# Kernel tuning notes

Measured on AMD Instinct MI355X. Metric: run time of the kernel, lower is better.

The kernel has to match this reference:

```python
import jax, jax.numpy as jnp
import numpy as np

B, T, F, D, HD = 16, 512, 16, 256, 256


def _init(k, shape, fan_in):
    return (jax.random.uniform(k, shape, minval=-1.0, maxval=1.0) / np.sqrt(fan_in)).astype(jnp.float32)


def setup_inputs() -> dict:
    key = jax.random.key(0)
    ks = jax.random.split(key, 16)
    return {
        "x": jax.random.normal(ks[0], (B, T, F), dtype=jnp.float32),
        # per-variable encoder params, batched over F (Linear(1,D) + GRN(D,HD,D))
        "w1": _init(ks[1], (F, D), 1), "b1": _init(ks[2], (F, D), 1),
        "fc1_w": _init(ks[3], (F, D, HD), D), "fc1_b": _init(ks[4], (F, HD), D),
        "fc2_w": _init(ks[5], (F, HD, D), HD), "fc2_b": _init(ks[6], (F, D), HD),
        "glu_w": _init(ks[7], (F, D, 2 * D), D), "glu_b": _init(ks[8], (F, 2 * D), D),
        "ln_g": jnp.ones((F, D), jnp.float32), "ln_b": jnp.zeros((F, D), jnp.float32),
        # weight GRN(F, HD, F); skip is Identity since d_in == d_out
        "wg_fc1_w": _init(ks[9], (F, HD), F), "wg_fc1_b": _init(ks[10], (HD,), F),
        "wg_fc2_w": _init(ks[11], (HD, F), HD), "wg_fc2_b": _init(ks[12], (F,), HD),
        "wg_glu_w": _init(ks[13], (F, 2 * F), F), "wg_glu_b": _init(ks[14], (2 * F,), F),
        "wg_ln_g": jnp.ones((F,), jnp.float32), "wg_ln_b": jnp.zeros((F,), jnp.float32),
    }


def _layernorm(x, g, b, eps=1e-5):
    m = jnp.mean(x, axis=-1, keepdims=True)
    v = jnp.var(x, axis=-1, keepdims=True)
    return (x - m) * jax.lax.rsqrt(v + eps) * g + b


def reference(x, w1, b1, fc1_w, fc1_b, fc2_w, fc2_b, glu_w, glu_b, ln_g, ln_b,
              wg_fc1_w, wg_fc1_b, wg_fc2_w, wg_fc2_b, wg_glu_w, wg_glu_b,
              wg_ln_g, wg_ln_b):
    # --- per-variable towers, batched over F (dropout is identity at eval) ---
    h0 = jax.nn.relu(x[..., None] * w1 + b1)                       # [B,T,F,D]
    y = jax.nn.elu(jnp.einsum('btfd,fdh->btfh', h0, fc1_w) + fc1_b)
    y = jnp.einsum('btfh,fhd->btfd', y, fc2_w) + fc2_b
    g = jnp.einsum('btfd,fde->btfe', y, glu_w) + glu_b             # [B,T,F,2D]
    a, gate = jnp.split(g, 2, axis=-1)
    H = _layernorm(h0 + a * jax.nn.sigmoid(gate), ln_g, ln_b)      # [B,T,F,D]
    # --- variable-weight GRN (time_distributed=True) ---
    yw = jax.nn.elu(x @ wg_fc1_w + wg_fc1_b)
    yw = yw @ wg_fc2_w + wg_fc2_b
    gw = x @ jnp.zeros((F, 0), x.dtype) if False else yw @ wg_glu_w + wg_glu_b
    aw, gatew = jnp.split(gw, 2, axis=-1)
    w = _layernorm(x + aw * jax.nn.sigmoid(gatew), wg_ln_g, wg_ln_b)
    w = jax.nn.softmax(w, axis=-1)                                 # [B,T,F]
    z = jnp.einsum('btfd,btf->btd', H, w)                          # [B,T,D]
    return z, w
```

## Files before the change

kernel.cpp:

```cpp
#include <hip/hip_runtime.h>
#include <hip/hip_bf16.h>

#define NBT 8192
#define NF  16
#define ND  256
#define NH  256
#define N2D 512

typedef short bf16x8 __attribute__((ext_vector_type(8)));
typedef float f32x4 __attribute__((ext_vector_type(4)));
typedef unsigned short u16x8 __attribute__((ext_vector_type(8)));

__device__ __forceinline__ float bf2f(unsigned short u) {
  return __uint_as_float(((unsigned)u) << 16);
}
__device__ __forceinline__ unsigned short f2bf(float f) {
  unsigned u = __float_as_uint(f);
  return (unsigned short)((u + 0x7FFFu + ((u >> 16) & 1u)) >> 16);
}

#define GLOAD16(src, dst)                                                     \
  __builtin_amdgcn_global_load_lds(                                           \
      (const __attribute__((address_space(1))) unsigned int*)(src),           \
      (__attribute__((address_space(3))) unsigned int*)(dst), 16, 0, 0)

__global__ __launch_bounds__(256) void wgrn_kernel(
    const float* __restrict__ x, const float* __restrict__ fw1,
    const float* __restrict__ fb1, const float* __restrict__ fw2,
    const float* __restrict__ fb2, const float* __restrict__ gwt,
    const float* __restrict__ gbt, const float* __restrict__ lng,
    const float* __restrict__ lnb, float* __restrict__ wout) {
  __shared__ float w1t[256 * 16];
  __shared__ float w2s[256 * 16];
  const int tid = threadIdx.x;
  for (int i = tid; i < 4096; i += 256) {
    int ff = i >> 8, j = i & 255;
    w1t[j * 16 + ff] = fw1[i];
    w2s[i] = fw2[i];
  }
  __syncthreads();
  const int sub  = tid & 7;
  const int rowi = tid >> 3;
  const int bt   = blockIdx.x * 32 + rowi;
  float xr[16];
#pragma unroll
  for (int i = 0; i < 4; ++i)
    *(float4*)&xr[i * 4] = *(const float4*)(x + (size_t)bt * 16 + i * 4);
  float acc2[16];
#pragma unroll
  for (int q = 0; q < 16; ++q) acc2[q] = 0.f;
  for (int j = sub; j < 256; j += 8) {
    float h = fb1[j];
    const float* wr = &w1t[j * 16];
#pragma unroll
    for (int q = 0; q < 16; ++q) h = fmaf(xr[q], wr[q], h);
    h = h > 0.f ? h : expm1f(h);
    const float* w2r = &w2s[j * 16];
#pragma unroll
    for (int q = 0; q < 16; ++q) acc2[q] = fmaf(h, w2r[q], acc2[q]);
  }
#pragma unroll
  for (int off = 1; off < 8; off <<= 1) {
#pragma unroll
    for (int q = 0; q < 16; ++q) acc2[q] += __shfl_xor(acc2[q], off);
  }
#pragma unroll
  for (int q = 0; q < 16; ++q) acc2[q] += fb2[q];
  float gw[32];
#pragma unroll
  for (int k = 0; k < 32; ++k) {
    float s = gbt[k];
#pragma unroll
    for (int q = 0; q < 16; ++q) s = fmaf(acc2[q], gwt[q * 32 + k], s);
    gw[k] = s;
  }
  float v[16];
  float mean = 0.f;
#pragma unroll
  for (int q = 0; q < 16; ++q) {
    float sg = 1.f / (1.f + __expf(-gw[16 + q]));
    v[q] = fmaf(gw[q], sg, xr[q]);
    mean += v[q];
  }
  mean *= (1.f / 16.f);
  float var = 0.f;
#pragma unroll
  for (int q = 0; q < 16; ++q) { float d = v[q] - mean; var = fmaf(d, d, var); }
  var *= (1.f / 16.f);
  float rstd = rsqrtf(var + 1e-5f);
  float mx = -1e30f;
#pragma unroll
  for (int q = 0; q < 16; ++q) {
    v[q] = (v[q] - mean) * rstd * lng[q] + lnb[q];
    mx = fmaxf(mx, v[q]);
  }
  float se = 0.f;
#pragma unroll
  for (int q = 0; q < 16; ++q) { v[q] = __expf(v[q] - mx); se += v[q]; }
  float inv = 1.f / se;
  if (sub == 0) {
#pragma unroll
    for (int i = 0; i < 4; ++i) {
      float4 o = { v[i*4+0]*inv, v[i*4+1]*inv, v[i*4+2]*inv, v[i*4+3]*inv };
      *(float4*)(wout + (size_t)bt * 16 + i * 4) = o;
    }
  }
}

__global__ void transpose_cast(const float* __restrict__ src,
                               unsigned short* __restrict__ dst, int K, int N) {
  __shared__ float tile[32][33];
  const int f = blockIdx.z;
  const float* s = src + (size_t)f * K * N;
  unsigned short* d = dst + (size_t)f * K * N;
  const int k0 = blockIdx.y * 32, n0 = blockIdx.x * 32;
  const int tx = threadIdx.x, ty = threadIdx.y;
#pragma unroll
  for (int i = 0; i < 32; i += 8)
    tile[ty + i][tx] = s[(size_t)(k0 + ty + i) * N + n0 + tx];
  __syncthreads();
#pragma unroll
  for (int i = 0; i < 32; i += 8)
    d[(size_t)(n0 + ty + i) * K + k0 + tx] = f2bf(tile[tx][ty + i]);
}

__global__ __launch_bounds__(256, 4) void g1_kernel(
    const float* __restrict__ x, const float* __restrict__ w1,
    const float* __restrict__ b1, const unsigned short* __restrict__ fc1t,
    const float* __restrict__ fc1_b, unsigned short* __restrict__ y1) {
  __shared__ __align__(16) char arena[34816];
  __shared__ float xw[128];
  unsigned short* abuf = (unsigned short*)arena;
  unsigned short* bbuf = (unsigned short*)(arena + 17408);
  unsigned short* cbuf = (unsigned short*)arena;
  const int tid = threadIdx.x, lane = tid & 63, wid = tid >> 6;
  const int rl = lane & 15, kc = lane >> 4;
  const int f = blockIdx.z, m0 = blockIdx.y * 128, n0 = blockIdx.x * 128;
  const unsigned short* Bf = fc1t + (size_t)f * NH * ND;
  const float* w1f = w1 + f * ND;
  const float* b1f = b1 + f * ND;
  if (tid < 128) xw[tid] = x[(size_t)(m0 + tid) * NF + f];
  const int wm = (wid >> 1) * 64, wn = (wid & 1) * 64;

  f32x4 acc[4][4];
#pragma unroll
  for (int m = 0; m < 4; ++m)
#pragma unroll
    for (int n = 0; n < 4; ++n) acc[m][n] = (f32x4){0.f, 0.f, 0.f, 0.f};

  for (int kt = 0; kt < ND; kt += 64) {
    __syncthreads();
#pragma unroll
    for (int i = 0; i < 4; ++i) {
      int s = tid + 256 * i;
      int row = s >> 3, sl = s & 7;
      const unsigned short* gb =
          Bf + (size_t)(n0 + row) * ND + kt + ((sl ^ (row & 7)) << 3);
      GLOAD16(gb, (char*)bbuf + (wid * 64 + 256 * i) * 16);
    }
#pragma unroll
    for (int i = 0; i < 4; ++i) {
      int vi = tid + 256 * i;
      int row = vi >> 3, c8 = vi & 7, c = kt + c8 * 8;
      float xv = xw[row];
      float4 wa = *(const float4*)(w1f + c);
      float4 wb = *(const float4*)(w1f + c + 4);
      float4 ba = *(const float4*)(b1f + c);
      float4 bb = *(const float4*)(b1f + c + 4);
      u16x8 o;
      o[0] = f2bf(fmaxf(fmaf(xv, wa.x, ba.x), 0.f));
      o[1] = f2bf(fmaxf(fmaf(xv, wa.y, ba.y), 0.f));
      o[2] = f2bf(fmaxf(fmaf(xv, wa.z, ba.z), 0.f));
      o[3] = f2bf(fmaxf(fmaf(xv, wa.w, ba.w), 0.f));
      o[4] = f2bf(fmaxf(fmaf(xv, wb.x, bb.x), 0.f));
      o[5] = f2bf(fmaxf(fmaf(xv, wb.y, bb.y), 0.f));
      o[6] = f2bf(fmaxf(fmaf(xv, wb.z, bb.z), 0.f));
      o[7] = f2bf(fmaxf(fmaf(xv, wb.w, bb.w), 0.f));
      *(u16x8*)(abuf + row * 68 + c8 * 8) = o;
    }
    __syncthreads();
#pragma unroll
    for (int kk = 0; kk < 2; ++kk) {
      bf16x8 av[4], bv[4];
      int s = kk * 4 + kc;
#pragma unroll
      for (int m = 0; m < 4; ++m) {
        int r = wm + m * 16 + rl;
        av[m] = *(const bf16x8*)(abuf + r * 68 + s * 8);
      }
#pragma unroll
      for (int n = 0; n < 4; ++n) {
        int rr = wn + n * 16 + rl;
        int ps = s ^ (rr & 7);
        bv[n] = *(const bf16x8*)((const char*)bbuf + rr * 128 + ps * 16);
      }
#pragma unroll
      for (int m = 0; m < 4; ++m)
#pragma unroll
        for (int n = 0; n < 4; ++n)
          acc[m][n] = __builtin_amdgcn_mfma_f32_16x16x32_bf16(av[m], bv[n],
                                                              acc[m][n], 0, 0, 0);
    }
  }

  __syncthreads();
  const int rq = lane >> 4;
#pragma unroll
  for (int n = 0; n < 4; ++n) {
    int cl = wn + n * 16 + rl;
    float bvv = fc1_b[f * NH + n0 + cl];
#pragma unroll
    for (int m = 0; m < 4; ++m) {
#pragma unroll
      for (int j = 0; j < 4; ++j) {
        int r = wm + m * 16 + rq * 4 + j;
        float v = acc[m][n][j] + bvv;
        v = v > 0.f ? v : expm1f(v);
        cbuf[r * 136 + cl] = f2bf(v);
      }
    }
  }
  __syncthreads();
#pragma unroll
  for (int v = 0; v < 8; ++v) {
    int row = (tid >> 4) + v * 16, chunk = tid & 15;
    u16x8 val = *(const u16x8*)(cbuf + row * 136 + chunk * 8);
    *(u16x8*)(y1 + ((size_t)f * NBT + m0 + row) * NH + n0 + chunk * 8) = val;
  }
}

__global__ __launch_bounds__(512, 4) void g2_kernel(
    const unsigned short* __restrict__ y1,
    const unsigned short* __restrict__ fc2t, const float* __restrict__ fc2_b,
    unsigned short* __restrict__ y2) {
  __shared__ __align__(16) char arena[49152];
  unsigned short* abuf = (unsigned short*)arena;
  unsigned short* bbuf = (unsigned short*)(arena + 16384);
  unsigned short* cbuf = (unsigned short*)arena;
  const int tid = threadIdx.x, lane = tid & 63, wid = tid >> 6;
  const int rl = lane & 15, kc = lane >> 4;
  const int f = blockIdx.y, m0 = blockIdx.x * 128;
  const unsigned short* Af = y1 + (size_t)f * NBT * NH;
  const unsigned short* Bf = fc2t + (size_t)f * ND * NH;
  const int wm = (wid >> 2) * 64, wn = (wid & 3) * 64;

  f32x4 acc[4][4];
#pragma unroll
  for (int m = 0; m < 4; ++m)
#pragma unroll
    for (int n = 0; n < 4; ++n) acc[m][n] = (f32x4){0.f, 0.f, 0.f, 0.f};

  for (int kt = 0; kt < NH; kt += 64) {
    __syncthreads();
#pragma unroll
    for (int i = 0; i < 2; ++i) {
      int s = tid + 512 * i;
      int row = s >> 3, sl = s & 7;
      const unsigned short* ga =
          Af + (size_t)(m0 + row) * NH + kt + ((sl ^ (row & 7)) << 3);
      GLOAD16(ga, (char*)abuf + (wid * 64 + 512 * i) * 16);
    }
#pragma unroll
    for (int i = 0; i < 4; ++i) {
      int s = tid + 512 * i;
      int row = s >> 3, sl = s & 7;
      const unsigned short* gb =
          Bf + (size_t)row * NH + kt + ((sl ^ (row & 7)) << 3);
      GLOAD16(gb, (char*)bbuf + (wid * 64 + 512 * i) * 16);
    }
    __syncthreads();
#pragma unroll
    for (int kk = 0; kk < 2; ++kk) {
      bf16x8 av[4], bv[4];
      int s = kk * 4 + kc;
#pragma unroll
      for (int m = 0; m < 4; ++m) {
        int r = wm + m * 16 + rl;
        int ps = s ^ (r & 7);
        av[m] = *(const bf16x8*)((const char*)abuf + r * 128 + ps * 16);
      }
#pragma unroll
      for (int n = 0; n < 4; ++n) {
        int rr = wn + n * 16 + rl;
        int ps = s ^ (rr & 7);
        bv[n] = *(const bf16x8*)((const char*)bbuf + rr * 128 + ps * 16);
      }
#pragma unroll
      for (int m = 0; m < 4; ++m)
#pragma unroll
        for (int n = 0; n < 4; ++n)
          acc[m][n] = __builtin_amdgcn_mfma_f32_16x16x32_bf16(av[m], bv[n],
                                                              acc[m][n], 0, 0, 0);
    }
  }

  const int rq = lane >> 4;
  const int hsel = (wid & 3) >> 1;
#pragma unroll
  for (int h = 0; h < 2; ++h) {
    __syncthreads();
    if (hsel == h) {
#pragma unroll
      for (int n = 0; n < 4; ++n) {
        int c = wn + n * 16 + rl;
        int cl = c - h * 128;
        float bvv = fc2_b[f * ND + c];
#pragma unroll
        for (int m = 0; m < 4; ++m) {
#pragma unroll
          for (int j = 0; j < 4; ++j) {
            int r = wm + m * 16 + rq * 4 + j;
            cbuf[r * 136 + cl] = f2bf(acc[m][n][j] + bvv);
          }
        }
      }
    }
    __syncthreads();
#pragma unroll
    for (int v = 0; v < 4; ++v) {
      int row = (tid >> 4) + v * 32, chunk = tid & 15;
      u16x8 val = *(const u16x8*)(cbuf + row * 136 + chunk * 8);
      *(u16x8*)(y2 + ((size_t)f * NBT + m0 + row) * ND + h * 128 + chunk * 8) =
          val;
    }
  }
}

__global__ __launch_bounds__(512, 4) void g3_kernel(
    const unsigned short* __restrict__ y2,
    const unsigned short* __restrict__ glut, const float* __restrict__ glu_b,
    const float* __restrict__ x, const float* __restrict__ w1,
    const float* __restrict__ b1, const float* __restrict__ ln_g,
    const float* __restrict__ ln_b, unsigned short* __restrict__ H) {
  __shared__ __align__(16) char arena[73728];
  __shared__ float xw[64];
  __shared__ float2 sums[8][64];
  __shared__ float2 sums2[64];
  unsigned short* abuf = (unsigned short*)arena;
  unsigned short* bbuf = (unsigned short*)(arena + 8192);
  unsigned short* vbuf = (unsigned short*)arena;

  const int tid = threadIdx.x, lane = tid & 63, wid = tid >> 6;
  const int rl = lane & 15, rq = lane >> 4;
  const int f = blockIdx.y, m0 = blockIdx.x * 64;
  const unsigned short* Af = y2 + (size_t)f * NBT * ND;
  const unsigned short* Bf = glut + (size_t)f * ND * N2D;
  const float* w1f = w1 + f * ND;
  const float* b1f = b1 + f * ND;
  const int colb = wid * 32;
  if (tid < 64) xw[tid] = x[(size_t)(m0 + tid) * NF + f];

  f32x4 acc[4][4];
#pragma unroll
  for (int m = 0; m < 4; ++m)
#pragma unroll
    for (int n = 0; n < 4; ++n) acc[m][n] = (f32x4){0.f, 0.f, 0.f, 0.f};

  for (int kt = 0; kt < ND; kt += 64) {
    __syncthreads();
    {
      int s = tid;
      int row = s >> 3, sl = s & 7;
      const unsigned short* ga =
          Af + (size_t)(m0 + row) * ND + kt + ((sl ^ (row & 7)) << 3);
      GLOAD16(ga, (char*)abuf + (wid * 64) * 16);
    }
#pragma unroll
    for (int i = 0; i < 8; ++i) {
      int s = tid + 512 * i;
      int row = s >> 3, sl = s & 7;
      const unsigned short* gb =
          Bf + (size_t)row * ND + kt + ((sl ^ (row & 7)) << 3);
      GLOAD16(gb, (char*)bbuf + (wid * 64 + 512 * i) * 16);
    }
    __syncthreads();
#pragma unroll
    for (int kk = 0; kk < 2; ++kk) {
      bf16x8 av[4], bv[4];
      int s = kk * 4 + rq;
#pragma unroll
      for (int m = 0; m < 4; ++m) {
        int r = m * 16 + rl;
        int ps = s ^ (r & 7);
        av[m] = *(const bf16x8*)((const char*)abuf + r * 128 + ps * 16);
      }
#pragma unroll
      for (int n = 0; n < 4; ++n) {
        int rr = (n < 2) ? (colb + n * 16 + rl)
                         : (256 + colb + (n - 2) * 16 + rl);
        int ps = s ^ (rr & 7);
        bv[n] = *(const bf16x8*)((const char*)bbuf + rr * 128 + ps * 16);
      }
#pragma unroll
      for (int m = 0; m < 4; ++m)
#pragma unroll
        for (int n = 0; n < 4; ++n)
          acc[m][n] = __builtin_amdgcn_mfma_f32_16x16x32_bf16(av[m], bv[n],
                                                              acc[m][n], 0, 0, 0);
    }
  }

#pragma unroll
  for (int n = 0; n < 2; ++n) {
    int cA = colb + n * 16 + rl;
    float ab_ = glu_b[f * N2D + cA];
    float gb_ = glu_b[f * N2D + 256 + cA];
    float w1c = w1f[cA], b1c = b1f[cA];
#pragma unroll
    for (int m = 0; m < 4; ++m) {
#pragma unroll
      for (int j = 0; j < 4; ++j) {
        int r = m * 16 + rq * 4 + j;
        float a = acc[m][n][j] + ab_;
        float g = acc[m][n + 2][j] + gb_;
        float sg = 1.f / (1.f + __expf(-g));
        float h0 = fmaxf(fmaf(xw[r], w1c, b1c), 0.f);
        acc[m][n][j] = fmaf(a, sg, h0);
      }
    }
  }
#pragma unroll
  for (int m = 0; m < 4; ++m) {
#pragma unroll
    for (int j = 0; j < 4; ++j) {
      float s = acc[m][0][j] + acc[m][1][j];
      float q = fmaf(acc[m][0][j], acc[m][0][j],
                     acc[m][1][j] * acc[m][1][j]);
#pragma unroll
      for (int off = 1; off < 16; off <<= 1) {
        s += __shfl_xor(s, off);
        q += __shfl_xor(q, off);
      }
      if (rl == 0) sums[wid][m * 16 + rq * 4 + j] = make_float2(s, q);
    }
  }
  __syncthreads();
  if (tid < 64) {
    float tot = 0.f, tot2 = 0.f;
#pragma unroll
    for (int wv = 0; wv < 8; ++wv) {
      float2 p = sums[wv][tid];
      tot += p.x;
      tot2 += p.y;
    }
    float mean = tot * (1.f / 256.f);
    float var  = tot2 * (1.f / 256.f) - mean * mean;
    sums2[tid] = make_float2(mean, rsqrtf(var + 1e-5f));
  }
  __syncthreads();
#pragma unroll
  for (int n = 0; n < 2; ++n) {
    int cA = colb + n * 16 + rl;
    float lg = ln_g[f * ND + cA], lb = ln_b[f * ND + cA];
#pragma unroll
    for (int m = 0; m < 4; ++m) {
#pragma unroll
      for (int j = 0; j < 4; ++j) {
        int r = m * 16 + rq * 4 + j;
        float2 mr = sums2[r];
        vbuf[r * 264 + cA] = f2bf(fmaf((acc[m][n][j] - mr.x) * mr.y, lg, lb));
      }
    }
  }
  __syncthreads();
  {
    int row = tid >> 3, chunk = tid & 7;
    unsigned short* Hrow = H + ((size_t)f * NBT + m0 + row) * ND;
#pragma unroll
    for (int v = 0; v < 4; ++v) {
      u16x8 val = *(const u16x8*)(vbuf + row * 264 + chunk * 8 + v * 64);
      *(u16x8*)(Hrow + chunk * 8 + v * 64) = val;
    }
  }
}

__global__ __launch_bounds__(256) void combine_kernel(
    const unsigned short* __restrict__ H, const float* __restrict__ w,
    float* __restrict__ z) {
  int idx = blockIdx.x * 256 + threadIdx.x;
  int bt = idx >> 5;
  int d  = (idx & 31) << 3;
  float a[8];
#pragma unroll
  for (int j = 0; j < 8; ++j) a[j] = 0.f;
#pragma unroll
  for (int f = 0; f < 16; ++f) {
    u16x8 hv = *(const u16x8*)(H + ((size_t)f * NBT + bt) * ND + d);
    float wvv = w[bt * 16 + f];
#pragma unroll
    for (int j = 0; j < 8; ++j) a[j] = fmaf(bf2f(hv[j]), wvv, a[j]);
  }
  float4 o0 = {a[0], a[1], a[2], a[3]};
  float4 o1 = {a[4], a[5], a[6], a[7]};
  *(float4*)(z + (size_t)bt * ND + d)     = o0;
  *(float4*)(z + (size_t)bt * ND + d + 4) = o1;
}

extern "C" void kernel_launch(void* const* d_in, const int* in_sizes, int n_in,
                              void* d_out, int out_size, void* d_ws,
                              size_t ws_size, hipStream_t stream) {
  const float* x        = (const float*)d_in[0];
  const float* w1       = (const float*)d_in[1];
  const float* b1       = (const float*)d_in[2];
  const float* fc1_w    = (const float*)d_in[3];
  const float* fc1_b    = (const float*)d_in[4];
  const float* fc2_w    = (const float*)d_in[5];
  const float* fc2_b    = (const float*)d_in[6];
  const float* glu_w    = (const float*)d_in[7];
  const float* glu_b    = (const float*)d_in[8];
  const float* ln_g     = (const float*)d_in[9];
  const float* ln_b     = (const float*)d_in[10];
  const float* wg_fc1_w = (const float*)d_in[11];
  const float* wg_fc1_b = (const float*)d_in[12];
  const float* wg_fc2_w = (const float*)d_in[13];
  const float* wg_fc2_b = (const float*)d_in[14];
  const float* wg_glu_w = (const float*)d_in[15];
  const float* wg_glu_b = (const float*)d_in[16];
  const float* wg_ln_g  = (const float*)d_in[17];
  const float* wg_ln_b  = (const float*)d_in[18];

  char* ws = (char*)d_ws;
  unsigned short* fc1t = (unsigned short*)ws;
  unsigned short* fc2t = fc1t + (size_t)NF * NH * ND;
  unsigned short* glut = fc2t + (size_t)NF * ND * NH;
  unsigned short* y1   = (unsigned short*)(ws + (8ull << 20));
  unsigned short* y2   = (unsigned short*)(ws + (72ull << 20));
  unsigned short* Hbuf = (unsigned short*)(ws + (136ull << 20));

  float* zout = (float*)d_out;
  float* wout = zout + (size_t)NBT * ND;

  wgrn_kernel<<<256, 256, 0, stream>>>(x, wg_fc1_w, wg_fc1_b, wg_fc2_w,
                                       wg_fc2_b, wg_glu_w, wg_glu_b, wg_ln_g,
                                       wg_ln_b, wout);
  transpose_cast<<<dim3(8, 8, NF),  dim3(32, 8), 0, stream>>>(fc1_w, fc1t, ND, NH);
  transpose_cast<<<dim3(8, 8, NF),  dim3(32, 8), 0, stream>>>(fc2_w, fc2t, NH, ND);
  transpose_cast<<<dim3(16, 8, NF), dim3(32, 8), 0, stream>>>(glu_w, glut, ND, N2D);

  g1_kernel<<<dim3(NH / 128, NBT / 128, NF), 256, 0, stream>>>(
      x, w1, b1, fc1t, fc1_b, y1);
  g2_kernel<<<dim3(NBT / 128, NF), 512, 0, stream>>>(y1, fc2t, fc2_b, y2);
  g3_kernel<<<dim3(NBT / 64, NF), 512, 0, stream>>>(y2, glut, glu_b, x, w1, b1,
                                                    ln_g, ln_b, Hbuf);
  combine_kernel<<<(NBT * ND / 8) / 256, 256, 0, stream>>>(Hbuf, wout, zout);

  (void)in_sizes; (void)n_in; (void)out_size; (void)ws_size;
}
```

Before: 232.1 us.

## Double-buffer LDS tiles in GEMM kernels and merge weight transpose launches

Restructures the K loops of the three per-variable GEMM kernels into a two-stage ping-pong pipeline. The next tile's global-to-LDS loads (and, in g1, the h0 recompute) are issued before the MFMAs on the current tile, which also removes one barrier per iteration. The aim is to hide global load latency behind compute. In exchange the LDS footprint doubles (up to about 147KB in g3), which cuts how many blocks fit per CU and lowers the launch_bounds occupancy hints. The three weight transpose/cast launches are merged into one kernel to save launch overhead, at the cost of some duplicated or idle blocks.

```diff
diff --git a/kernel.cpp b/kernel.cpp
--- a/kernel.cpp
+++ b/kernel.cpp
@@ -107,13 +107,26 @@
   }
 }
 
-__global__ void transpose_cast(const float* __restrict__ src,
-                               unsigned short* __restrict__ dst, int K, int N) {
+__global__ void transpose_all(const float* __restrict__ fc1_w,
+                              const float* __restrict__ fc2_w,
+                              const float* __restrict__ glu_w,
+                              unsigned short* __restrict__ fc1t,
+                              unsigned short* __restrict__ fc2t,
+                              unsigned short* __restrict__ glut) {
   __shared__ float tile[32][33];
-  const int f = blockIdx.z;
+  const int which = blockIdx.z >> 4;
+  const int f     = blockIdx.z & 15;
+  const float* src;
+  unsigned short* dst;
+  int K, N, bx = blockIdx.x;
+  if (which == 0)      { src = fc1_w; dst = fc1t; K = ND; N = NH; }
+  else if (which == 1) { src = fc2_w; dst = fc2t; K = NH; N = ND; }
+  else                 { src = glu_w; dst = glut; K = ND; N = N2D;
+                         bx += (which == 3) ? 8 : 0; }
+  if (bx * 32 >= N) return;
   const float* s = src + (size_t)f * K * N;
   unsigned short* d = dst + (size_t)f * K * N;
-  const int k0 = blockIdx.y * 32, n0 = blockIdx.x * 32;
+  const int k0 = blockIdx.y * 32, n0 = bx * 32;
   const int tx = threadIdx.x, ty = threadIdx.y;
 #pragma unroll
   for (int i = 0; i < 32; i += 8)
@@ -124,23 +137,25 @@
     d[(size_t)(n0 + ty + i) * K + k0 + tx] = f2bf(tile[tx][ty + i]);
 }
 
-__global__ __launch_bounds__(256, 4) void g1_kernel(
+__global__ __launch_bounds__(256, 2) void g1_kernel(
     const float* __restrict__ x, const float* __restrict__ w1,
     const float* __restrict__ b1, const unsigned short* __restrict__ fc1t,
     const float* __restrict__ fc1_b, unsigned short* __restrict__ y1) {
-  __shared__ __align__(16) char arena[34816];
+  __shared__ __align__(16) char arena[67584];
   __shared__ float xw[128];
-  unsigned short* abuf = (unsigned short*)arena;
-  unsigned short* bbuf = (unsigned short*)(arena + 17408);
-  unsigned short* cbuf = (unsigned short*)arena;
+  unsigned short* abufs = (unsigned short*)arena;
+  unsigned short* bbufs = (unsigned short*)(arena + 34816);
+  unsigned short* cbuf  = (unsigned short*)arena;
   const int tid = threadIdx.x, lane = tid & 63, wid = tid >> 6;
   const int rl = lane & 15, kc = lane >> 4;
   const int f = blockIdx.z, m0 = blockIdx.y * 128, n0 = blockIdx.x * 128;
   const unsigned short* Bf = fc1t + (size_t)f * NH * ND;
   const float* w1f = w1 + f * ND;
   const float* b1f = b1 + f * ND;
+  const int wm = (wid >> 1) * 64, wn = (wid & 1) * 64;
+
   if (tid < 128) xw[tid] = x[(size_t)(m0 + tid) * NF + f];
-  const int wm = (wid >> 1) * 64, wn = (wid & 1) * 64;
+  __syncthreads();
 
   f32x4 acc[4][4];
 #pragma unroll
@@ -148,16 +163,19 @@
 #pragma unroll
     for (int n = 0; n < 4; ++n) acc[m][n] = (f32x4){0.f, 0.f, 0.f, 0.f};
 
-  for (int kt = 0; kt < ND; kt += 64) {
-    __syncthreads();
+  auto stage_B = [&](int kt, int buf) {
+    unsigned short* bb = bbufs + buf * (128 * 64);
 #pragma unroll
     for (int i = 0; i < 4; ++i) {
       int s = tid + 256 * i;
       int row = s >> 3, sl = s & 7;
       const unsigned short* gb =
           Bf + (size_t)(n0 + row) * ND + kt + ((sl ^ (row & 7)) << 3);
-      GLOAD16(gb, (char*)bbuf + (wid * 64 + 256 * i) * 16);
-    }
+      GLOAD16(gb, (char*)bb + (wid * 64 + 256 * i) * 16);
+    }
+  };
+  auto stage_h0 = [&](int kt, int buf) {
+    unsigned short* ab = abufs + buf * (128 * 68);
 #pragma unroll
     for (int i = 0; i < 4; ++i) {
       int vi = tid + 256 * i;
@@ -166,19 +184,22 @@
       float4 wa = *(const float4*)(w1f + c);
       float4 wb = *(const float4*)(w1f + c + 4);
       float4 ba = *(const float4*)(b1f + c);
-      float4 bb = *(const float4*)(b1f + c + 4);
+      float4 bb2 = *(const float4*)(b1f + c + 4);
       u16x8 o;
       o[0] = f2bf(fmaxf(fmaf(xv, wa.x, ba.x), 0.f));
       o[1] = f2bf(fmaxf(fmaf(xv, wa.y, ba.y), 0.f));
       o[2] = f2bf(fmaxf(fmaf(xv, wa.z, ba.z), 0.f));
       o[3] = f2bf(fmaxf(fmaf(xv, wa.w, ba.w), 0.f));
-      o[4] = f2bf(fmaxf(fmaf(xv, wb.x, bb.x), 0.f));
-      o[5] = f2bf(fmaxf(fmaf(xv, wb.y, bb.y), 0.f));
-      o[6] = f2bf(fmaxf(fmaf(xv, wb.z, bb.z), 0.f));
-      o[7] = f2bf(fmaxf(fmaf(xv, wb.w, bb.w), 0.f));
-      *(u16x8*)(abuf + row * 68 + c8 * 8) = o;
-    }
-    __syncthreads();
+      o[4] = f2bf(fmaxf(fmaf(xv, wb.x, bb2.x), 0.f));
+      o[5] = f2bf(fmaxf(fmaf(xv, wb.y, bb2.y), 0.f));
+      o[6] = f2bf(fmaxf(fmaf(xv, wb.z, bb2.z), 0.f));
+      o[7] = f2bf(fmaxf(fmaf(xv, wb.w, bb2.w), 0.f));
+      *(u16x8*)(ab + row * 68 + c8 * 8) = o;
+    }
+  };
+  auto compute = [&](int buf) {
+    const unsigned short* ab = abufs + buf * (128 * 68);
+    const unsigned short* bb = bbufs + buf * (128 * 64);
 #pragma unroll
     for (int kk = 0; kk < 2; ++kk) {
       bf16x8 av[4], bv[4];
@@ -186,13 +207,13 @@
 #pragma unroll
       for (int m = 0; m < 4; ++m) {
         int r = wm + m * 16 + rl;
-        av[m] = *(const bf16x8*)(abuf + r * 68 + s * 8);
+        av[m] = *(const bf16x8*)(ab + r * 68 + s * 8);
       }
 #pragma unroll
       for (int n = 0; n < 4; ++n) {
         int rr = wn + n * 16 + rl;
         int ps = s ^ (rr & 7);
-        bv[n] = *(const bf16x8*)((const char*)bbuf + rr * 128 + ps * 16);
+        bv[n] = *(const bf16x8*)((const char*)bb + rr * 128 + ps * 16);
       }
 #pragma unroll
       for (int m = 0; m < 4; ++m)
@@ -201,9 +222,20 @@
           acc[m][n] = __builtin_amdgcn_mfma_f32_16x16x32_bf16(av[m], bv[n],
                                                               acc[m][n], 0, 0, 0);
     }
-  }
-
-  __syncthreads();
+  };
+
+  stage_B(0, 0);
+  stage_h0(0, 0);
+  __syncthreads();
+#pragma unroll
+  for (int t = 0; t < 4; ++t) {
+    int cur = t & 1;
+    if (t < 3) stage_B((t + 1) * 64, cur ^ 1);
+    compute(cur);
+    if (t < 3) stage_h0((t + 1) * 64, cur ^ 1);
+    __syncthreads();
+  }
+
   const int rq = lane >> 4;
 #pragma unroll
   for (int n = 0; n < 4; ++n) {
@@ -229,14 +261,14 @@
   }
 }
 
-__global__ __launch_bounds__(512, 4) void g2_kernel(
+__global__ __launch_bounds__(512, 2) void g2_kernel(
     const unsigned short* __restrict__ y1,
     const unsigned short* __restrict__ fc2t, const float* __restrict__ fc2_b,
     unsigned short* __restrict__ y2) {
-  __shared__ __align__(16) char arena[49152];
-  unsigned short* abuf = (unsigned short*)arena;
-  unsigned short* bbuf = (unsigned short*)(arena + 16384);
-  unsigned short* cbuf = (unsigned short*)arena;
+  __shared__ __align__(16) char arena[98304];
+  unsigned short* abufs = (unsigned short*)arena;
+  unsigned short* bbufs = (unsigned short*)(arena + 32768);
+  unsigned short* cbuf  = (unsigned short*)arena;
   const int tid = threadIdx.x, lane = tid & 63, wid = tid >> 6;
   const int rl = lane & 15, kc = lane >> 4;
   const int f = blockIdx.y, m0 = blockIdx.x * 128;
@@ -250,15 +282,16 @@
 #pragma unroll
     for (int n = 0; n < 4; ++n) acc[m][n] = (f32x4){0.f, 0.f, 0.f, 0.f};
 
-  for (int kt = 0; kt < NH; kt += 64) {
-    __syncthreads();
+  auto stage = [&](int kt, int buf) {
+    unsigned short* ab = abufs + buf * (128 * 64);
+    unsigned short* bb = bbufs + buf * (256 * 64);
 #pragma unroll
     for (int i = 0; i < 2; ++i) {
       int s = tid + 512 * i;
       int row = s >> 3, sl = s & 7;
       const unsigned short* ga =
           Af + (size_t)(m0 + row) * NH + kt + ((sl ^ (row & 7)) << 3);
-      GLOAD16(ga, (char*)abuf + (wid * 64 + 512 * i) * 16);
+      GLOAD16(ga, (char*)ab + (wid * 64 + 512 * i) * 16);
     }
 #pragma unroll
     for (int i = 0; i < 4; ++i) {
@@ -266,9 +299,12 @@
       int row = s >> 3, sl = s & 7;
       const unsigned short* gb =
           Bf + (size_t)row * NH + kt + ((sl ^ (row & 7)) << 3);
-      GLOAD16(gb, (char*)bbuf + (wid * 64 + 512 * i) * 16);
-    }
-    __syncthreads();
+      GLOAD16(gb, (char*)bb + (wid * 64 + 512 * i) * 16);
+    }
+  };
+  auto compute = [&](int buf) {
+    const unsigned short* ab = abufs + buf * (128 * 64);
+    const unsigned short* bb = bbufs + buf * (256 * 64);
 #pragma unroll
     for (int kk = 0; kk < 2; ++kk) {
       bf16x8 av[4], bv[4];
@@ -277,13 +313,13 @@
       for (int m = 0; m < 4; ++m) {
         int r = wm + m * 16 + rl;
         int ps = s ^ (r & 7);
-        av[m] = *(const bf16x8*)((const char*)abuf + r * 128 + ps * 16);
+        av[m] = *(const bf16x8*)((const char*)ab + r * 128 + ps * 16);
       }
 #pragma unroll
       for (int n = 0; n < 4; ++n) {
         int rr = wn + n * 16 + rl;
         int ps = s ^ (rr & 7);
-        bv[n] = *(const bf16x8*)((const char*)bbuf + rr * 128 + ps * 16);
+        bv[n] = *(const bf16x8*)((const char*)bb + rr * 128 + ps * 16);
       }
 #pragma unroll
       for (int m = 0; m < 4; ++m)
@@ -292,13 +328,23 @@
           acc[m][n] = __builtin_amdgcn_mfma_f32_16x16x32_bf16(av[m], bv[n],
                                                               acc[m][n], 0, 0, 0);
     }
+  };
+
+  stage(0, 0);
+  __syncthreads();
+#pragma unroll
+  for (int t = 0; t < 4; ++t) {
+    int cur = t & 1;
+    if (t < 3) stage((t + 1) * 64, cur ^ 1);
+    compute(cur);
+    __syncthreads();
   }
 
   const int rq = lane >> 4;
   const int hsel = (wid & 3) >> 1;
 #pragma unroll
   for (int h = 0; h < 2; ++h) {
-    __syncthreads();
+    if (h) __syncthreads();
     if (hsel == h) {
 #pragma unroll
       for (int n = 0; n < 4; ++n) {
@@ -326,19 +372,19 @@
   }
 }
 
-__global__ __launch_bounds__(512, 4) void g3_kernel(
+__global__ __launch_bounds__(512, 2) void g3_kernel(
     const unsigned short* __restrict__ y2,
     const unsigned short* __restrict__ glut, const float* __restrict__ glu_b,
     const float* __restrict__ x, const float* __restrict__ w1,
     const float* __restrict__ b1, const float* __restrict__ ln_g,
     const float* __restrict__ ln_b, unsigned short* __restrict__ H) {
-  __shared__ __align__(16) char arena[73728];
+  __shared__ __align__(16) char arena[147456];
   __shared__ float xw[64];
   __shared__ float2 sums[8][64];
   __shared__ float2 sums2[64];
-  unsigned short* abuf = (unsigned short*)arena;
-  unsigned short* bbuf = (unsigned short*)(arena + 8192);
-  unsigned short* vbuf = (unsigned short*)arena;
+  unsigned short* abufs = (unsigned short*)arena;
+  unsigned short* bbufs = (unsigned short*)(arena + 16384);
+  unsigned short* vbuf  = (unsigned short*)arena;
 
   const int tid = threadIdx.x, lane = tid & 63, wid = tid >> 6;
   const int rl = lane & 15, rq = lane >> 4;
@@ -356,14 +402,15 @@
 #pragma unroll
     for (int n = 0; n < 4; ++n) acc[m][n] = (f32x4){0.f, 0.f, 0.f, 0.f};
 
-  for (int kt = 0; kt < ND; kt += 64) {
-    __syncthreads();
+  auto stage = [&](int kt, int buf) {
+    unsigned short* ab = abufs + buf * (64 * 64);
+    unsigned short* bb = bbufs + buf * (512 * 64);
     {
       int s = tid;
       int row = s >> 3, sl = s & 7;
       const unsigned short* ga =
           Af + (size_t)(m0 + row) * ND + kt + ((sl ^ (row & 7)) << 3);
-      GLOAD16(ga, (char*)abuf + (wid * 64) * 16);
+      GLOAD16(ga, (char*)ab + (wid * 64) * 16);
     }
 #pragma unroll
     for (int i = 0; i < 8; ++i) {
@@ -371,9 +418,12 @@
       int row = s >> 3, sl = s & 7;
       const unsigned short* gb =
           Bf + (size_t)row * ND + kt + ((sl ^ (row & 7)) << 3);
-      GLOAD16(gb, (char*)bbuf + (wid * 64 + 512 * i) * 16);
-    }
-    __syncthreads();
+      GLOAD16(gb, (char*)bb + (wid * 64 + 512 * i) * 16);
+    }
+  };
+  auto compute = [&](int buf) {
+    const unsigned short* ab = abufs + buf * (64 * 64);
+    const unsigned short* bb = bbufs + buf * (512 * 64);
 #pragma unroll
     for (int kk = 0; kk < 2; ++kk) {
       bf16x8 av[4], bv[4];
@@ -382,14 +432,14 @@
       for (int m = 0; m < 4; ++m) {
         int r = m * 16 + rl;
         int ps = s ^ (r & 7);
-        av[m] = *(const bf16x8*)((const char*)abuf + r * 128 + ps * 16);
+        av[m] = *(const bf16x8*)((const char*)ab + r * 128 + ps * 16);
       }
 #pragma unroll
       for (int n = 0; n < 4; ++n) {
         int rr = (n < 2) ? (colb + n * 16 + rl)
                          : (256 + colb + (n - 2) * 16 + rl);
         int ps = s ^ (rr & 7);
-        bv[n] = *(const bf16x8*)((const char*)bbuf + rr * 128 + ps * 16);
+        bv[n] = *(const bf16x8*)((const char*)bb + rr * 128 + ps * 16);
       }
 #pragma unroll
       for (int m = 0; m < 4; ++m)
@@ -398,6 +448,16 @@
           acc[m][n] = __builtin_amdgcn_mfma_f32_16x16x32_bf16(av[m], bv[n],
                                                               acc[m][n], 0, 0, 0);
     }
+  };
+
+  stage(0, 0);
+  __syncthreads();
+#pragma unroll
+  for (int t = 0; t < 4; ++t) {
+    int cur = t & 1;
+    if (t < 3) stage((t + 1) * 64, cur ^ 1);
+    compute(cur);
+    __syncthreads();
   }
 
 #pragma unroll
@@ -533,9 +593,8 @@
   wgrn_kernel<<<256, 256, 0, stream>>>(x, wg_fc1_w, wg_fc1_b, wg_fc2_w,
                                        wg_fc2_b, wg_glu_w, wg_glu_b, wg_ln_g,
                                        wg_ln_b, wout);
-  transpose_cast<<<dim3(8, 8, NF),  dim3(32, 8), 0, stream>>>(fc1_w, fc1t, ND, NH);
-  transpose_cast<<<dim3(8, 8, NF),  dim3(32, 8), 0, stream>>>(fc2_w, fc2t, NH, ND);
-  transpose_cast<<<dim3(16, 8, NF), dim3(32, 8), 0, stream>>>(glu_w, glut, ND, N2D);
+  transpose_all<<<dim3(16, 8, 64), dim3(32, 8), 0, stream>>>(
+      fc1_w, fc2_w, glu_w, fc1t, fc2t, glut);
 
   g1_kernel<<<dim3(NH / 128, NBT / 128, NF), 256, 0, stream>>>(
       x, w1, b1, fc1t, fc1_b, y1);
```

After: 269.7 us. 1.16x slower.
